# Optimization experiments

Measured on AMD Instinct MI355X. Metric: run time of the kernel, lower is better.

The kernel has to match this reference:

```python
import jax, jax.numpy as jnp
import numpy as np

WIN = 7  # window size (w1 = w2 = 7)

def _rel_pos_indices(w: int) -> jnp.ndarray:
    # Matches RelPosBias 2-D branch: [(w*w), (w*w)] indices into (2w-1)^2 table
    p = np.arange(w)
    gi, gj = np.meshgrid(p, p, indexing='ij')
    grid = np.stack([gi.reshape(-1), gj.reshape(-1)], axis=-1)  # [w*w, 2]
    rel = grid[:, None, :] - grid[None, :, :]                   # [w*w, w*w, 2]
    rel = rel + (w - 1)
    idx = rel[..., 0] * (2 * w - 1) + rel[..., 1]               # [w*w, w*w]
    return jnp.asarray(idx, dtype=jnp.int32)


def setup_inputs() -> dict:
    key = jax.random.key(0)
    k1, k2, k3, k4 = jax.random.split(key, 4)
    dim, heads = 256, 8
    b, gx, gy = 64, 8, 8
    x = jax.random.normal(k1, (b, gx, gy, WIN, WIN, dim), dtype=jnp.float32)
    # torch nn.Linear weight layout: [out_features, in_features]
    w_qkv = jax.random.normal(k2, (3 * dim, dim), dtype=jnp.float32) * (dim ** -0.5)
    w_out = jax.random.normal(k3, (dim, dim), dtype=jnp.float32) * (dim ** -0.5)
    rel_emb = jax.random.normal(k4, ((2 * WIN - 1) ** 2, heads), dtype=jnp.float32) * 0.02
    rel_idx = _rel_pos_indices(WIN)
    return {"x": x, "w_qkv": w_qkv, "w_out": w_out, "rel_emb": rel_emb, "rel_idx": rel_idx}


def reference(x, w_qkv, w_out, rel_emb, rel_idx):
    b, gx, gy, w1, w2, d = x.shape
    h = rel_emb.shape[1]          # heads
    dh = d // h                    # dim_head
    scale = dh ** -0.5
    n = w1 * w2                    # tokens per window (49)

    xr = x.reshape(b * gx * gy, n, d)                        # (B, n, d)
    qkv = jnp.einsum('bnd,ed->bne', xr, w_qkv)               # (B, n, 3d)
    q, k, v = jnp.split(qkv, 3, axis=-1)
    split_heads = lambda t: t.reshape(t.shape[0], n, h, dh).transpose(0, 2, 1, 3)
    q, k, v = map(split_heads, (q, k, v))                    # (B, h, n, dh)

    sim = jnp.einsum('bhid,bhjd->bhij', q * scale, k)        # (B, h, n, n)
    bias = rel_emb[rel_idx]                                   # (n, n, h)
    sim = sim + bias.transpose(2, 0, 1)[None]                 # + (1, h, n, n)
    attn = jax.nn.softmax(sim, axis=-1)

    out = jnp.einsum('bhij,bhjd->bhid', attn, v)              # (B, h, n, dh)
    out = out.transpose(0, 2, 1, 3).reshape(-1, w1, w2, d)    # (B, w1, w2, d)
    out = jnp.einsum('bxyd,ed->bxye', out, w_out)
    return out.reshape(b, gx, gy, w1, w2, d)
```

## Files before the change

### kernel.cpp

```cpp
#include <hip/hip_runtime.h>
#include <hip/hip_bf16.h>

typedef __bf16 bf16x8 __attribute__((ext_vector_type(8)));
typedef __bf16 bf16x4v __attribute__((ext_vector_type(4)));
typedef float f32x4 __attribute__((ext_vector_type(4)));

#define MFMA(a, b, c) __builtin_amdgcn_mfma_f32_16x16x32_bf16((a), (b), (c), 0, 0, 0)
#define NEG_BIG (-1e30f)

#define QK_LD 36
#define VT_LD 72
#define P_LD 68
#define K_OFF 0
#define VT_OFF 2304
#define Q_OFF 4608
#define P_OFF 6912
#define TOTAL_ELS 11264

static __device__ inline bf16x8 ld8x2(const __bf16* p) {
  bf16x4v lo = *(const bf16x4v*)p;
  bf16x4v hi = *(const bf16x4v*)(p + 4);
  bf16x8 r;
  r[0] = lo[0]; r[1] = lo[1]; r[2] = lo[2]; r[3] = lo[3];
  r[4] = hi[0]; r[5] = hi[1]; r[6] = hi[2]; r[7] = hi[3];
  return r;
}

__global__ __launch_bounds__(256) void prep_kernel(
    const float* __restrict__ w_qkv, const float* __restrict__ w_out,
    const float* __restrict__ rel_emb, const int* __restrict__ rel_idx,
    __bf16* __restrict__ wqkv_f, __bf16* __restrict__ wout_f,
    float* __restrict__ bias) {
  const float kScale = 0.17677669529663687f;
  int idx = blockIdx.x * 256 + threadIdx.x;
  if (idx < 24576) {
    int lane = idx & 63, k2 = (idx >> 6) & 7;
    int hn = idx >> 9;
    int nt = hn % 6, h = hn / 6;
    int quad = lane >> 4, l16 = lane & 15;
    int grow = (nt >> 1) * 256 + h * 32 + (nt & 1) * 16 + l16;
    const float* src = w_qkv + grow * 256 + k2 * 32 + quad * 8;
    float s = (nt < 2) ? kScale : 1.0f;
    bf16x8 d;
#pragma unroll
    for (int j = 0; j < 8; ++j) d[j] = (__bf16)(src[j] * s);
    *(bf16x8*)&wqkv_f[idx * 8] = d;
  } else if (idx < 32768) {
    int j2 = idx - 24576;
    int lane = j2 & 63, kk = (j2 >> 6) & 7, ntile = j2 >> 9;
    int quad = lane >> 4, l16 = lane & 15;
    const float* src = w_out + (ntile * 16 + l16) * 256 + kk * 32 + quad * 8;
    bf16x8 d;
#pragma unroll
    for (int j = 0; j < 8; ++j) d[j] = (__bf16)src[j];
    *(bf16x8*)&wout_f[j2 * 8] = d;
  } else if (idx < 65536) {
    int j = idx - 32768;
    int h = j >> 12;
    int mt = (j >> 10) & 3;
    int nt = (j >> 8) & 3;
    int lane = (j >> 2) & 63;
    int r = j & 3;
    int row = mt * 16 + ((lane >> 4) << 2) + r;
    int col = nt * 16 + (lane & 15);
    float v = NEG_BIG;
    if (row < 49 && col < 49) v = rel_emb[rel_idx[row * 49 + col] * 8 + h];
    bias[j] = v;
  }
}

__global__ __launch_bounds__(256, 4) void attn_kernel(
    const float* __restrict__ x, const __bf16* __restrict__ wqkv,
    const __bf16* __restrict__ wout, const float* __restrict__ bias,
    float* __restrict__ out) {
  __shared__ __attribute__((aligned(16))) __bf16 sm[TOTAL_ELS];

  const int tid = threadIdx.x;
  const int wave = tid >> 6;
  const int lane = tid & 63;
  const int quad = lane >> 4;
  const int l16 = lane & 15;
  const int i0 = wave * 16 + quad * 4;
  const int am = wave * 16 + l16;

  const f32x4 fzero = {0.f, 0.f, 0.f, 0.f};

  bf16x8 afr[8];
  {
    const float* xrow =
        x + (size_t)blockIdx.x * 12544 + (am > 48 ? 48 : am) * 256;
#pragma unroll
    for (int k2 = 0; k2 < 8; ++k2) {
      const float* xp = xrow + k2 * 32 + quad * 8;
      float4 v0 = *(const float4*)xp;
      float4 v1 = *(const float4*)(xp + 4);
      bf16x8 a;
      a[0] = (__bf16)v0.x; a[1] = (__bf16)v0.y; a[2] = (__bf16)v0.z; a[3] = (__bf16)v0.w;
      a[4] = (__bf16)v1.x; a[5] = (__bf16)v1.y; a[6] = (__bf16)v1.z; a[7] = (__bf16)v1.w;
      afr[k2] = a;
    }
  }

  bf16x8 ofr[8];

#pragma unroll
  for (int h = 0; h < 8; ++h) {
    f32x4 acc[6];
#pragma unroll
    for (int t = 0; t < 6; ++t) acc[t] = fzero;
    {
      const __bf16* wb = wqkv + (size_t)h * 24576;
#pragma unroll
      for (int k2 = 0; k2 < 8; ++k2) {
        bf16x8 a = afr[k2];
#pragma unroll
        for (int nt = 0; nt < 6; ++nt) {
          bf16x8 b = *(const bf16x8*)&wb[(nt * 8 + k2) * 512 + lane * 8];
          acc[nt] = MFMA(a, b, acc[nt]);
        }
      }
    }

    if (h) __syncthreads();

#pragma unroll
    for (int t = 0; t < 2; ++t) {
#pragma unroll
      for (int r = 0; r < 4; ++r) {
        sm[Q_OFF + (i0 + r) * QK_LD + t * 16 + l16] = (__bf16)acc[t][r];
        sm[K_OFF + (i0 + r) * QK_LD + t * 16 + l16] = (__bf16)acc[2 + t][r];
      }
      bf16x4v pv;
#pragma unroll
      for (int r = 0; r < 4; ++r) pv[r] = (__bf16)acc[4 + t][r];
      *(bf16x4v*)&sm[VT_OFF + (t * 16 + l16) * VT_LD + i0] = pv;
    }

    f32x4 sim[4];
    {
      const float* bb = bias + (h << 12) + (wave << 10) + (lane << 2);
#pragma unroll
      for (int nt = 0; nt < 4; ++nt) sim[nt] = *(const f32x4*)&bb[nt << 8];
    }
    __syncthreads();

    {
      bf16x8 a = ld8x2(&sm[Q_OFF + am * QK_LD + quad * 8]);
#pragma unroll
      for (int nt = 0; nt < 4; ++nt) {
        bf16x8 b = ld8x2(&sm[K_OFF + (nt * 16 + l16) * QK_LD + quad * 8]);
        sim[nt] = MFMA(a, b, sim[nt]);
      }
    }

#pragma unroll
    for (int r = 0; r < 4; ++r) {
      float e0 = __expf(sim[0][r]), e1 = __expf(sim[1][r]);
      float e2 = __expf(sim[2][r]), e3 = __expf(sim[3][r]);
      float sum = e0 + e1 + e2 + e3;
      sum += __shfl_xor(sum, 1);
      sum += __shfl_xor(sum, 2);
      sum += __shfl_xor(sum, 4);
      sum += __shfl_xor(sum, 8);
      float rs = (sum > 0.f) ? (1.0f / sum) : 0.f;
      int row = i0 + r;
      sm[P_OFF + row * P_LD + l16] = (__bf16)(e0 * rs);
      sm[P_OFF + row * P_LD + 16 + l16] = (__bf16)(e1 * rs);
      sm[P_OFF + row * P_LD + 32 + l16] = (__bf16)(e2 * rs);
      sm[P_OFF + row * P_LD + 48 + l16] = (__bf16)(e3 * rs);
    }

    f32x4 oa[2];
    oa[0] = fzero;
    oa[1] = fzero;
#pragma unroll
    for (int kk = 0; kk < 2; ++kk) {
      bf16x8 a = ld8x2(&sm[P_OFF + am * P_LD + kk * 32 + quad * 8]);
#pragma unroll
      for (int t = 0; t < 2; ++t) {
        bf16x8 b = *(const bf16x8*)&sm[VT_OFF + (t * 16 + l16) * VT_LD + kk * 32 + quad * 8];
        oa[t] = MFMA(a, b, oa[t]);
      }
    }
#pragma unroll
    for (int t = 0; t < 2; ++t)
#pragma unroll
      for (int r = 0; r < 4; ++r)
        sm[P_OFF + (i0 + r) * P_LD + t * 16 + l16] = (__bf16)oa[t][r];
    ofr[h] = ld8x2(&sm[P_OFF + am * P_LD + quad * 8]);
  }

  float* ob_base = out + (size_t)blockIdx.x * 12544;
  for (int ct = 0; ct < 8; ++ct) {
    f32x4 fa[2];
    fa[0] = fzero;
    fa[1] = fzero;
#pragma unroll
    for (int kk = 0; kk < 8; ++kk) {
#pragma unroll
      for (int t = 0; t < 2; ++t) {
        bf16x8 bw = *(const bf16x8*)&wout[((ct * 2 + t) * 8 + kk) * 512 + lane * 8];
        fa[t] = MFMA(ofr[kk], bw, fa[t]);
      }
    }
    float* ob = ob_base + ct * 32;
#pragma unroll
    for (int t = 0; t < 2; ++t)
#pragma unroll
      for (int r = 0; r < 4; ++r) {
        int row = i0 + r;
        if (row < 49) ob[row * 256 + t * 16 + l16] = fa[t][r];
      }
  }
}

extern "C" void kernel_launch(void* const* d_in, const int* in_sizes, int n_in,
                              void* d_out, int out_size, void* d_ws, size_t ws_size,
                              hipStream_t stream) {
  (void)in_sizes; (void)n_in; (void)out_size; (void)ws_size;
  const float* x = (const float*)d_in[0];
  const float* w_qkv = (const float*)d_in[1];
  const float* w_out = (const float*)d_in[2];
  const float* rel_emb = (const float*)d_in[3];
  const int* rel_idx = (const int*)d_in[4];
  float* out = (float*)d_out;

  char* ws = (char*)d_ws;
  __bf16* wqkv_f = (__bf16*)ws;
  __bf16* wout_f = (__bf16*)(ws + 393216);
  float* bias = (float*)(ws + 524288);

  prep_kernel<<<256, 256, 0, stream>>>(w_qkv, w_out, rel_emb, rel_idx,
                                       wqkv_f, wout_f, bias);
  attn_kernel<<<4096, 256, 0, stream>>>(x, wqkv_f, wout_f, bias, out);
}
```

Before: 750.2 us.

## Assign heads to waves instead of row tiles to remove per-head block barriers

Previously each of the four waves owned 16 token rows and the block looped over all 8 heads together, with two __syncthreads per head. Now each wave owns two whole heads across all 64 rows. It does the QKV projection, attention and PV for each head in a private LDS region with no block barriers, then exchanges head outputs through shared memory once before the output projection. This removes the per-head barriers and lets each wave reuse a weight fragment across 4 row tiles. The cost is larger register arrays (acc[4][6], sim[4][4]), bigger LDS, occupancy lowered to 2 blocks per CU, and x re-read from global per head.

```diff
diff --git a/kernel.cpp b/kernel.cpp
--- a/kernel.cpp
+++ b/kernel.cpp
@@ -11,11 +11,14 @@
 #define QK_LD 36
 #define VT_LD 72
 #define P_LD 68
-#define K_OFF 0
-#define VT_OFF 2304
-#define Q_OFF 4608
-#define P_OFF 6912
-#define TOTAL_ELS 11264
+#define XO_LD 264
+#define RQ 0
+#define RK 2304
+#define RV 4608
+#define RP 0
+#define RD 6912
+#define WREG 8960
+#define TOTAL_ELS (4 * WREG)
 
 static __device__ inline bf16x8 ld8x2(const __bf16* p) {
   bf16x4v lo = *(const bf16x4v*)p;
@@ -69,7 +72,7 @@
   }
 }
 
-__global__ __launch_bounds__(256, 4) void attn_kernel(
+__global__ __launch_bounds__(256, 2) void attn_kernel(
     const float* __restrict__ x, const __bf16* __restrict__ wqkv,
     const __bf16* __restrict__ wout, const float* __restrict__ bias,
     float* __restrict__ out) {
@@ -80,115 +83,166 @@
   const int lane = tid & 63;
   const int quad = lane >> 4;
   const int l16 = lane & 15;
+
+  const f32x4 fzero = {0.f, 0.f, 0.f, 0.f};
+  __bf16* mw = sm + wave * WREG;
+  const float* xg = x + (size_t)blockIdx.x * 12544;
+
+  f32x4 oa1[4][2];
+
+#pragma unroll
+  for (int hh = 0; hh < 2; ++hh) {
+    const int h = wave + hh * 4;
+    const __bf16* wb = wqkv + (size_t)h * 24576;
+
+    f32x4 acc[4][6];
+#pragma unroll
+    for (int mt = 0; mt < 4; ++mt)
+#pragma unroll
+      for (int nt = 0; nt < 6; ++nt) acc[mt][nt] = fzero;
+
+#pragma unroll
+    for (int k2 = 0; k2 < 8; ++k2) {
+      bf16x8 a[4];
+#pragma unroll
+      for (int mt = 0; mt < 4; ++mt) {
+        const int row = (mt == 3) ? 48 : (mt * 16 + l16);
+        const float* xp = xg + row * 256 + k2 * 32 + quad * 8;
+        float4 v0 = *(const float4*)xp;
+        float4 v1 = *(const float4*)(xp + 4);
+        bf16x8 t;
+        t[0] = (__bf16)v0.x; t[1] = (__bf16)v0.y; t[2] = (__bf16)v0.z; t[3] = (__bf16)v0.w;
+        t[4] = (__bf16)v1.x; t[5] = (__bf16)v1.y; t[6] = (__bf16)v1.z; t[7] = (__bf16)v1.w;
+        a[mt] = t;
+      }
+#pragma unroll
+      for (int nt = 0; nt < 6; ++nt) {
+        bf16x8 b = *(const bf16x8*)&wb[(nt * 8 + k2) * 512 + lane * 8];
+#pragma unroll
+        for (int mt = 0; mt < 4; ++mt) acc[mt][nt] = MFMA(a[mt], b, acc[mt][nt]);
+      }
+    }
+
+#pragma unroll
+    for (int mt = 0; mt < 4; ++mt) {
+      const int rb = mt * 16 + quad * 4;
+#pragma unroll
+      for (int t = 0; t < 2; ++t) {
+#pragma unroll
+        for (int r = 0; r < 4; ++r) {
+          mw[RQ + (rb + r) * QK_LD + t * 16 + l16] = (__bf16)acc[mt][t][r];
+          mw[RK + (rb + r) * QK_LD + t * 16 + l16] = (__bf16)acc[mt][2 + t][r];
+        }
+        bf16x4v pv;
+#pragma unroll
+        for (int r = 0; r < 4; ++r) pv[r] = (__bf16)acc[mt][4 + t][r];
+        *(bf16x4v*)&mw[RV + (t * 16 + l16) * VT_LD + rb] = pv;
+      }
+    }
+
+    f32x4 sim[4][4];
+    const float* bb = bias + (h << 12) + (lane << 2);
+#pragma unroll
+    for (int mt = 0; mt < 4; ++mt)
+#pragma unroll
+      for (int nt = 0; nt < 4; ++nt)
+        sim[mt][nt] = *(const f32x4*)&bb[(mt * 4 + nt) << 8];
+
+    bf16x8 aq[4];
+#pragma unroll
+    for (int mt = 0; mt < 4; ++mt)
+      aq[mt] = ld8x2(&mw[RQ + (mt * 16 + l16) * QK_LD + quad * 8]);
+#pragma unroll
+    for (int nt = 0; nt < 4; ++nt) {
+      bf16x8 bk = ld8x2(&mw[RK + (nt * 16 + l16) * QK_LD + quad * 8]);
+#pragma unroll
+      for (int mt = 0; mt < 4; ++mt) sim[mt][nt] = MFMA(aq[mt], bk, sim[mt][nt]);
+    }
+
+#pragma unroll
+    for (int mt = 0; mt < 4; ++mt) {
+      const int rb = mt * 16 + quad * 4;
+#pragma unroll
+      for (int r = 0; r < 4; ++r) {
+        float e0 = __expf(sim[mt][0][r]), e1 = __expf(sim[mt][1][r]);
+        float e2 = __expf(sim[mt][2][r]), e3 = __expf(sim[mt][3][r]);
+        float sum = e0 + e1 + e2 + e3;
+        sum += __shfl_xor(sum, 1);
+        sum += __shfl_xor(sum, 2);
+        sum += __shfl_xor(sum, 4);
+        sum += __shfl_xor(sum, 8);
+        float rs = (sum > 0.f) ? (1.0f / sum) : 0.f;
+        const int row = rb + r;
+        mw[RP + row * P_LD + l16] = (__bf16)(e0 * rs);
+        mw[RP + row * P_LD + 16 + l16] = (__bf16)(e1 * rs);
+        mw[RP + row * P_LD + 32 + l16] = (__bf16)(e2 * rs);
+        mw[RP + row * P_LD + 48 + l16] = (__bf16)(e3 * rs);
+      }
+    }
+
+    f32x4 po[4][2];
+#pragma unroll
+    for (int mt = 0; mt < 4; ++mt) {
+      po[mt][0] = fzero;
+      po[mt][1] = fzero;
+    }
+#pragma unroll
+    for (int kk = 0; kk < 2; ++kk) {
+      bf16x8 bv[2];
+#pragma unroll
+      for (int t = 0; t < 2; ++t)
+        bv[t] = *(const bf16x8*)&mw[RV + (t * 16 + l16) * VT_LD + kk * 32 + quad * 8];
+#pragma unroll
+      for (int mt = 0; mt < 4; ++mt) {
+        bf16x8 ap = ld8x2(&mw[RP + (mt * 16 + l16) * P_LD + kk * 32 + quad * 8]);
+#pragma unroll
+        for (int t = 0; t < 2; ++t) po[mt][t] = MFMA(ap, bv[t], po[mt][t]);
+      }
+    }
+
+    if (hh == 0) {
+#pragma unroll
+      for (int mt = 0; mt < 4; ++mt)
+#pragma unroll
+        for (int t = 0; t < 2; ++t) {
+          bf16x4v d;
+#pragma unroll
+          for (int r = 0; r < 4; ++r) d[r] = (__bf16)po[mt][t][r];
+          *(bf16x4v*)&mw[RD + lane * 32 + mt * 8 + t * 4] = d;
+        }
+    } else {
+#pragma unroll
+      for (int mt = 0; mt < 4; ++mt)
+#pragma unroll
+        for (int t = 0; t < 2; ++t) oa1[mt][t] = po[mt][t];
+    }
+  }
+
+  bf16x8 or0[4];
+#pragma unroll
+  for (int mt = 0; mt < 4; ++mt)
+    or0[mt] = *(const bf16x8*)&mw[RD + lane * 32 + mt * 8];
+  __syncthreads();
+#pragma unroll
+  for (int mt = 0; mt < 4; ++mt) {
+    const int rb = mt * 16 + quad * 4;
+#pragma unroll
+    for (int t = 0; t < 2; ++t)
+#pragma unroll
+      for (int r = 0; r < 4; ++r) {
+        sm[(rb + r) * XO_LD + wave * 32 + t * 16 + l16] = or0[mt][t * 4 + r];
+        sm[(rb + r) * XO_LD + (wave + 4) * 32 + t * 16 + l16] =
+            (__bf16)oa1[mt][t][r];
+      }
+  }
+  __syncthreads();
+
+  const int am = wave * 16 + l16;
   const int i0 = wave * 16 + quad * 4;
-  const int am = wave * 16 + l16;
-
-  const f32x4 fzero = {0.f, 0.f, 0.f, 0.f};
-
-  bf16x8 afr[8];
-  {
-    const float* xrow =
-        x + (size_t)blockIdx.x * 12544 + (am > 48 ? 48 : am) * 256;
-#pragma unroll
-    for (int k2 = 0; k2 < 8; ++k2) {
-      const float* xp = xrow + k2 * 32 + quad * 8;
-      float4 v0 = *(const float4*)xp;
-      float4 v1 = *(const float4*)(xp + 4);
-      bf16x8 a;
-      a[0] = (__bf16)v0.x; a[1] = (__bf16)v0.y; a[2] = (__bf16)v0.z; a[3] = (__bf16)v0.w;
-      a[4] = (__bf16)v1.x; a[5] = (__bf16)v1.y; a[6] = (__bf16)v1.z; a[7] = (__bf16)v1.w;
-      afr[k2] = a;
-    }
-  }
-
   bf16x8 ofr[8];
-
-#pragma unroll
-  for (int h = 0; h < 8; ++h) {
-    f32x4 acc[6];
-#pragma unroll
-    for (int t = 0; t < 6; ++t) acc[t] = fzero;
-    {
-      const __bf16* wb = wqkv + (size_t)h * 24576;
-#pragma unroll
-      for (int k2 = 0; k2 < 8; ++k2) {
-        bf16x8 a = afr[k2];
-#pragma unroll
-        for (int nt = 0; nt < 6; ++nt) {
-          bf16x8 b = *(const bf16x8*)&wb[(nt * 8 + k2) * 512 + lane * 8];
-          acc[nt] = MFMA(a, b, acc[nt]);
-        }
-      }
-    }
-
-    if (h) __syncthreads();
-
-#pragma unroll
-    for (int t = 0; t < 2; ++t) {
-#pragma unroll
-      for (int r = 0; r < 4; ++r) {
-        sm[Q_OFF + (i0 + r) * QK_LD + t * 16 + l16] = (__bf16)acc[t][r];
-        sm[K_OFF + (i0 + r) * QK_LD + t * 16 + l16] = (__bf16)acc[2 + t][r];
-      }
-      bf16x4v pv;
-#pragma unroll
-      for (int r = 0; r < 4; ++r) pv[r] = (__bf16)acc[4 + t][r];
-      *(bf16x4v*)&sm[VT_OFF + (t * 16 + l16) * VT_LD + i0] = pv;
-    }
-
-    f32x4 sim[4];
-    {
-      const float* bb = bias + (h << 12) + (wave << 10) + (lane << 2);
-#pragma unroll
-      for (int nt = 0; nt < 4; ++nt) sim[nt] = *(const f32x4*)&bb[nt << 8];
-    }
-    __syncthreads();
-
-    {
-      bf16x8 a = ld8x2(&sm[Q_OFF + am * QK_LD + quad * 8]);
-#pragma unroll
-      for (int nt = 0; nt < 4; ++nt) {
-        bf16x8 b = ld8x2(&sm[K_OFF + (nt * 16 + l16) * QK_LD + quad * 8]);
-        sim[nt] = MFMA(a, b, sim[nt]);
-      }
-    }
-
-#pragma unroll
-    for (int r = 0; r < 4; ++r) {
-      float e0 = __expf(sim[0][r]), e1 = __expf(sim[1][r]);
-      float e2 = __expf(sim[2][r]), e3 = __expf(sim[3][r]);
-      float sum = e0 + e1 + e2 + e3;
-      sum += __shfl_xor(sum, 1);
-      sum += __shfl_xor(sum, 2);
-      sum += __shfl_xor(sum, 4);
-      sum += __shfl_xor(sum, 8);
-      float rs = (sum > 0.f) ? (1.0f / sum) : 0.f;
-      int row = i0 + r;
-      sm[P_OFF + row * P_LD + l16] = (__bf16)(e0 * rs);
-      sm[P_OFF + row * P_LD + 16 + l16] = (__bf16)(e1 * rs);
-      sm[P_OFF + row * P_LD + 32 + l16] = (__bf16)(e2 * rs);
-      sm[P_OFF + row * P_LD + 48 + l16] = (__bf16)(e3 * rs);
-    }
-
-    f32x4 oa[2];
-    oa[0] = fzero;
-    oa[1] = fzero;
-#pragma unroll
-    for (int kk = 0; kk < 2; ++kk) {
-      bf16x8 a = ld8x2(&sm[P_OFF + am * P_LD + kk * 32 + quad * 8]);
-#pragma unroll
-      for (int t = 0; t < 2; ++t) {
-        bf16x8 b = *(const bf16x8*)&sm[VT_OFF + (t * 16 + l16) * VT_LD + kk * 32 + quad * 8];
-        oa[t] = MFMA(a, b, oa[t]);
-      }
-    }
-#pragma unroll
-    for (int t = 0; t < 2; ++t)
-#pragma unroll
-      for (int r = 0; r < 4; ++r)
-        sm[P_OFF + (i0 + r) * P_LD + t * 16 + l16] = (__bf16)oa[t][r];
-    ofr[h] = ld8x2(&sm[P_OFF + am * P_LD + quad * 8]);
-  }
+#pragma unroll
+  for (int k8 = 0; k8 < 8; ++k8)
+    ofr[k8] = ld8x2(&sm[am * XO_LD + k8 * 32 + quad * 8]);
 
   float* ob_base = out + (size_t)blockIdx.x * 12544;
   for (int ct = 0; ct < 8; ++ct) {
@@ -208,7 +262,7 @@
     for (int t = 0; t < 2; ++t)
 #pragma unroll
       for (int r = 0; r < 4; ++r) {
-        int row = i0 + r;
+        const int row = i0 + r;
         if (row < 49) ob[row * 256 + t * 16 + l16] = fa[t][r];
       }
   }
```

Result: slower. 1.819 ms (+142.4%).

## Split output projection into separate kernel and double-buffer K/V in LDS

Applied to the files above, without the earlier changes.

The attention kernel now writes each head's bf16 output straight into the output buffer instead of holding all heads in registers. A new projection kernel reloads that bf16 buffer through shared memory and applies the output projection in place. K and V shared-memory buffers alternate between two slots so one barrier per head can be dropped, and launch bounds are raised to aim for higher occupancy. The cost is an extra kernel launch plus an extra global write and read of the intermediate activations.

```diff
diff --git a/kernel.cpp b/kernel.cpp
--- a/kernel.cpp
+++ b/kernel.cpp
@@ -11,11 +11,15 @@
 #define QK_LD 36
 #define VT_LD 72
 #define P_LD 68
-#define K_OFF 0
-#define VT_OFF 2304
-#define Q_OFF 4608
-#define P_OFF 6912
-#define TOTAL_ELS 11264
+#define RQ 0
+#define RK0 2304
+#define RK1 4608
+#define RV0 6912
+#define RV1 9216
+#define RP 11520
+#define TOTAL1 15872
+
+#define XO_LD 264
 
 static __device__ inline bf16x8 ld8x2(const __bf16* p) {
   bf16x4v lo = *(const bf16x4v*)p;
@@ -69,11 +73,10 @@
   }
 }
 
-__global__ __launch_bounds__(256, 4) void attn_kernel(
+__global__ __launch_bounds__(256, 5) void attn_kernel(
     const float* __restrict__ x, const __bf16* __restrict__ wqkv,
-    const __bf16* __restrict__ wout, const float* __restrict__ bias,
-    float* __restrict__ out) {
-  __shared__ __attribute__((aligned(16))) __bf16 sm[TOTAL_ELS];
+    const float* __restrict__ bias, float* __restrict__ out) {
+  __shared__ __attribute__((aligned(16))) __bf16 sm[TOTAL1];
 
   const int tid = threadIdx.x;
   const int wave = tid >> 6;
@@ -101,10 +104,13 @@
     }
   }
 
-  bf16x8 ofr[8];
+  __bf16* ob = (__bf16*)(out + (size_t)blockIdx.x * 12544);
 
 #pragma unroll
   for (int h = 0; h < 8; ++h) {
+    const int kb = (h & 1) ? RK1 : RK0;
+    const int vb = (h & 1) ? RV1 : RV0;
+
     f32x4 acc[6];
 #pragma unroll
     for (int t = 0; t < 6; ++t) acc[t] = fzero;
@@ -121,19 +127,17 @@
       }
     }
 
-    if (h) __syncthreads();
-
 #pragma unroll
     for (int t = 0; t < 2; ++t) {
 #pragma unroll
       for (int r = 0; r < 4; ++r) {
-        sm[Q_OFF + (i0 + r) * QK_LD + t * 16 + l16] = (__bf16)acc[t][r];
-        sm[K_OFF + (i0 + r) * QK_LD + t * 16 + l16] = (__bf16)acc[2 + t][r];
+        sm[RQ + (i0 + r) * QK_LD + t * 16 + l16] = (__bf16)acc[t][r];
+        sm[kb + (i0 + r) * QK_LD + t * 16 + l16] = (__bf16)acc[2 + t][r];
       }
       bf16x4v pv;
 #pragma unroll
       for (int r = 0; r < 4; ++r) pv[r] = (__bf16)acc[4 + t][r];
-      *(bf16x4v*)&sm[VT_OFF + (t * 16 + l16) * VT_LD + i0] = pv;
+      *(bf16x4v*)&sm[vb + (t * 16 + l16) * VT_LD + i0] = pv;
     }
 
     f32x4 sim[4];
@@ -145,10 +149,10 @@
     __syncthreads();
 
     {
-      bf16x8 a = ld8x2(&sm[Q_OFF + am * QK_LD + quad * 8]);
+      bf16x8 a = ld8x2(&sm[RQ + am * QK_LD + quad * 8]);
 #pragma unroll
       for (int nt = 0; nt < 4; ++nt) {
-        bf16x8 b = ld8x2(&sm[K_OFF + (nt * 16 + l16) * QK_LD + quad * 8]);
+        bf16x8 b = ld8x2(&sm[kb + (nt * 16 + l16) * QK_LD + quad * 8]);
         sim[nt] = MFMA(a, b, sim[nt]);
       }
     }
@@ -164,10 +168,10 @@
       sum += __shfl_xor(sum, 8);
       float rs = (sum > 0.f) ? (1.0f / sum) : 0.f;
       int row = i0 + r;
-      sm[P_OFF + row * P_LD + l16] = (__bf16)(e0 * rs);
-      sm[P_OFF + row * P_LD + 16 + l16] = (__bf16)(e1 * rs);
-      sm[P_OFF + row * P_LD + 32 + l16] = (__bf16)(e2 * rs);
-      sm[P_OFF + row * P_LD + 48 + l16] = (__bf16)(e3 * rs);
+      sm[RP + row * P_LD + l16] = (__bf16)(e0 * rs);
+      sm[RP + row * P_LD + 16 + l16] = (__bf16)(e1 * rs);
+      sm[RP + row * P_LD + 32 + l16] = (__bf16)(e2 * rs);
+      sm[RP + row * P_LD + 48 + l16] = (__bf16)(e3 * rs);
     }
 
     f32x4 oa[2];
@@ -175,22 +179,60 @@
     oa[1] = fzero;
 #pragma unroll
     for (int kk = 0; kk < 2; ++kk) {
-      bf16x8 a = ld8x2(&sm[P_OFF + am * P_LD + kk * 32 + quad * 8]);
+      bf16x8 a = ld8x2(&sm[RP + am * P_LD + kk * 32 + quad * 8]);
 #pragma unroll
       for (int t = 0; t < 2; ++t) {
-        bf16x8 b = *(const bf16x8*)&sm[VT_OFF + (t * 16 + l16) * VT_LD + kk * 32 + quad * 8];
+        bf16x8 b = *(const bf16x8*)&sm[vb + (t * 16 + l16) * VT_LD + kk * 32 + quad * 8];
         oa[t] = MFMA(a, b, oa[t]);
       }
     }
+
 #pragma unroll
     for (int t = 0; t < 2; ++t)
 #pragma unroll
-      for (int r = 0; r < 4; ++r)
-        sm[P_OFF + (i0 + r) * P_LD + t * 16 + l16] = (__bf16)oa[t][r];
-    ofr[h] = ld8x2(&sm[P_OFF + am * P_LD + quad * 8]);
-  }
-
-  float* ob_base = out + (size_t)blockIdx.x * 12544;
+      for (int r = 0; r < 4; ++r) {
+        int row = i0 + r;
+        if (row < 49) ob[row * 256 + h * 32 + t * 16 + l16] = (__bf16)oa[t][r];
+      }
+  }
+}
+
+__global__ __launch_bounds__(256, 4) void proj_kernel(
+    const __bf16* __restrict__ wout, float* __restrict__ out) {
+  __shared__ __attribute__((aligned(16))) __bf16 so[64 * XO_LD];
+
+  const int tid = threadIdx.x;
+  const int wave = tid >> 6;
+  const int lane = tid & 63;
+  const int quad = lane >> 4;
+  const int l16 = lane & 15;
+  const int i0 = wave * 16 + quad * 4;
+  const int am = wave * 16 + l16;
+
+  const f32x4 fzero = {0.f, 0.f, 0.f, 0.f};
+  float* outw = out + (size_t)blockIdx.x * 12544;
+  const __bf16* ob = (const __bf16*)outw;
+
+  for (int i = tid; i < 1568; i += 256) {
+    int row = i >> 5, c = (i & 31) * 8;
+    *(bf16x8*)&so[row * XO_LD + c] = *(const bf16x8*)&ob[row * 256 + c];
+  }
+  {
+    bf16x8 z;
+#pragma unroll
+    for (int j = 0; j < 8; ++j) z[j] = (__bf16)0.0f;
+    for (int i = tid; i < 480; i += 256) {
+      int row = 49 + (i >> 5), c = (i & 31) * 8;
+      *(bf16x8*)&so[row * XO_LD + c] = z;
+    }
+  }
+  __syncthreads();
+
+  bf16x8 ofr[8];
+#pragma unroll
+  for (int k8 = 0; k8 < 8; ++k8)
+    ofr[k8] = ld8x2(&so[am * XO_LD + k8 * 32 + quad * 8]);
+
   for (int ct = 0; ct < 8; ++ct) {
     f32x4 fa[2];
     fa[0] = fzero;
@@ -203,13 +245,13 @@
         fa[t] = MFMA(ofr[kk], bw, fa[t]);
       }
     }
-    float* ob = ob_base + ct * 32;
+    float* oc = outw + ct * 32;
 #pragma unroll
     for (int t = 0; t < 2; ++t)
 #pragma unroll
       for (int r = 0; r < 4; ++r) {
         int row = i0 + r;
-        if (row < 49) ob[row * 256 + t * 16 + l16] = fa[t][r];
+        if (row < 49) oc[row * 256 + t * 16 + l16] = fa[t][r];
       }
   }
 }
@@ -232,5 +274,6 @@
 
   prep_kernel<<<256, 256, 0, stream>>>(w_qkv, w_out, rel_emb, rel_idx,
                                        wqkv_f, wout_f, bias);
-  attn_kernel<<<4096, 256, 0, stream>>>(x, wqkv_f, wout_f, bias, out);
-}
+  attn_kernel<<<4096, 256, 0, stream>>>(x, wqkv_f, bias, out);
+  proj_kernel<<<4096, 256, 0, stream>>>(wout_f, out);
+}
```

Result: slower. 904.0 us (+20.5%).
